# Kernel tuning notes

Measured on AMD Instinct MI355X. Metric: run time of the kernel, lower is better.

Reference implementation:

```python
import jax, jax.numpy as jnp
import numpy as np

H, KV, HD = 16, 8, 128           # heads, kv heads, head_dim
THETA, EPS = 1.0e6, 1e-6         # rope theta, rmsnorm eps
QMAX = 127.0                     # symmetric int8


def qdq(x):
    """Symmetric int8 fake quant-dequant along last dim (per-token / per-out-channel)."""
    s = jnp.maximum(jnp.max(jnp.abs(x), axis=-1, keepdims=True) / QMAX, 1e-8)
    q = jnp.clip(jnp.round(x / s), -QMAX, QMAX) * s
    return x + jax.lax.stop_gradient(q - x)  # STE


def rms_norm(x, w):
    v = jnp.mean(jnp.square(x.astype(jnp.float32)), axis=-1, keepdims=True)
    return (x.astype(jnp.float32) * jax.lax.rsqrt(v + EPS)).astype(x.dtype) * w


def rotate_half(x):
    x1, x2 = jnp.split(x, 2, axis=-1)
    return jnp.concatenate([-x2, x1], axis=-1)


def setup_inputs() -> dict:
    key = jax.random.key(0)
    ks = jax.random.split(key, 6)
    B, S, D = 1, 2048, 2048
    return {
        "hidden_states": jax.random.normal(ks[0], (B, S, D), jnp.float32),
        "Wq": jax.random.normal(ks[1], (H * HD, D), jnp.float32) * 0.02,
        "Wk": jax.random.normal(ks[2], (KV * HD, D), jnp.float32) * 0.02,
        "Wv": jax.random.normal(ks[3], (KV * HD, D), jnp.float32) * 0.02,
        "Wo": jax.random.normal(ks[4], (D, H * HD), jnp.float32) * 0.02,
        "q_norm_w": jnp.ones((HD,), jnp.float32),
        "k_norm_w": jnp.ones((HD,), jnp.float32),
        "position_ids": jnp.arange(S, dtype=jnp.int32)[None, :],
    }


def reference(hidden_states, Wq, Wk, Wv, Wo, q_norm_w, k_norm_w, position_ids):
    B, S, D = hidden_states.shape
    xq = qdq(hidden_states)                                  # per-token act quant (shared input)
    q = (xq @ qdq(Wq).T).reshape(B, S, H, HD).transpose(0, 2, 1, 3)   # [B,H,S,hd]
    k = (xq @ qdq(Wk).T).reshape(B, S, KV, HD).transpose(0, 2, 1, 3)  # [B,KV,S,hd]
    v = (xq @ qdq(Wv).T).reshape(B, S, KV, HD).transpose(0, 2, 1, 3)

    q = rms_norm(q, q_norm_w)
    k = rms_norm(k, k_norm_w)

    # rotary embeddings
    inv = 1.0 / (THETA ** (jnp.arange(0, HD, 2, dtype=jnp.float32) / HD))
    freqs = position_ids.astype(jnp.float32)[..., None] * inv          # [B,S,hd/2]
    emb = jnp.concatenate([freqs, freqs], axis=-1)                     # [B,S,hd]
    cos = jnp.cos(emb)[:, None].astype(q.dtype)                        # [B,1,S,hd]
    sin = jnp.sin(emb)[:, None].astype(q.dtype)
    q = q * cos + rotate_half(q) * sin
    k = k * cos + rotate_half(k) * sin

    # qkt_matmul.quant_x1 / quant_x2
    q = qdq(q)
    k = qdq(k)

    # GQA repeat
    g = H // KV
    k = jnp.repeat(k, g, axis=1)
    v = jnp.repeat(v, g, axis=1)

    scores = jnp.einsum("bhqd,bhkd->bhqk", q, k) * (HD ** -0.5)       # [B,H,S,S]
    causal = jnp.tril(jnp.ones((S, S), bool))
    scores = jnp.where(causal[None, None], scores, jnp.float32(-1e9))
    p = jax.nn.softmax(scores.astype(jnp.float32), axis=-1).astype(q.dtype)

    # pv_matmul.quant_x1 / quant_x2
    p = qdq(p)
    v = qdq(v)
    attn = jnp.einsum("bhqk,bhkd->bhqd", p, v)                        # [B,H,S,hd]
    attn = attn.transpose(0, 2, 1, 3).reshape(B, S, H * HD)
    return qdq(attn) @ qdq(Wo).T
```

## Files before the change

### kernel.cpp

```cpp
#include <hip/hip_runtime.h>
#include <math.h>

#define NH 16
#define NKV 8
#define HDIM 128
#define SEQ 2048
#define DMODEL 2048

typedef int   v4i __attribute__((ext_vector_type(4)));
typedef float v4f __attribute__((ext_vector_type(4)));
typedef _Float16 v8h __attribute__((ext_vector_type(8)));

static constexpr float SM_SCALE = 0.08838834764831843f;

#define GLOBP(p) (__attribute__((address_space(1))) void*)(p)
#define LDSP(p)  (__attribute__((address_space(3))) void*)(p)
#define ASYNC16(g, l) __builtin_amdgcn_global_load_lds(GLOBP(g), LDSP(l), 16, 0, 0)


__device__ __forceinline__ unsigned short f2h_bits(float x) {
    _Float16 h = (_Float16)x;
    return __builtin_bit_cast(unsigned short, h);
}

__global__ __launch_bounds__(256) void quant_rope_k(const float* __restrict__ hidden,
        const float* __restrict__ Wq, const float* __restrict__ Wk,
        const float* __restrict__ Wv, const float* __restrict__ Wo,
        const int* __restrict__ pos_ids,
        signed char* __restrict__ out, float* __restrict__ scale,
        float* __restrict__ ct, float* __restrict__ st) {
    int p = blockIdx.x;
    if (p >= 512) {
        int t = (p - 512) * 4 + (threadIdx.x >> 6);
        int fi = threadIdx.x & 63;
        float inv = 1.0f / (float)pow(1.0e6, (double)fi / 64.0);
        float fr = (float)pos_ids[t] * inv;
        float sn, c;
        sincosf(fr, &sn, &c);
        ct[t * 64 + fi] = c;
        st[t * 64 + fi] = sn;
        return;
    }
    int row0g = p * 16;
    const float* in; int lr0;
    if (row0g < 2048)      { in = hidden; lr0 = row0g; }
    else if (row0g < 4096) { in = Wq; lr0 = row0g - 2048; }
    else if (row0g < 5120) { in = Wk; lr0 = row0g - 4096; }
    else if (row0g < 6144) { in = Wv; lr0 = row0g - 5120; }
    else                   { in = Wo; lr0 = row0g - 6144; }
    const int cols = 2048;
    int tid = threadIdx.x;
    __shared__ float srow[16];
    int r = tid >> 4, l16 = tid & 15;
    const float4* x4 = (const float4*)(in + (size_t)(lr0 + r) * cols);
    float amax = 0.f;
    for (int c4 = l16; c4 < (cols >> 2); c4 += 16) {
        float4 v = x4[c4];
        amax = fmaxf(amax, fmaxf(fmaxf(fabsf(v.x), fabsf(v.y)),
                                 fmaxf(fabsf(v.z), fabsf(v.w))));
    }
#pragma unroll
    for (int m = 1; m <= 8; m <<= 1) amax = fmaxf(amax, __shfl_xor(amax, m));
    if (l16 == 0) {
        float s = fmaxf(amax / 127.0f, 1e-8f);
        srow[r] = s;
        scale[row0g + r] = s;
    }
    __syncthreads();
    int total = (cols >> 4) * 16;
    size_t obase = (size_t)p * 32768;
    for (int idx = tid; idx < total; idx += 256) {
        int f = idx >> 6, q = (idx >> 4) & 3, rr = idx & 15;
        const float* src = in + (size_t)(lr0 + rr) * cols + f * 64 + q * 16;
        float s = srow[rr];
        unsigned int wds[4];
#pragma unroll
        for (int g = 0; g < 4; ++g) {
            float4 v = *(const float4*)(src + g * 4);
            int b0 = (int)fminf(fmaxf(rintf(v.x / s), -127.f), 127.f);
            int b1 = (int)fminf(fmaxf(rintf(v.y / s), -127.f), 127.f);
            int b2 = (int)fminf(fmaxf(rintf(v.z / s), -127.f), 127.f);
            int b3 = (int)fminf(fmaxf(rintf(v.w / s), -127.f), 127.f);
            wds[g] = (b0 & 255) | ((b1 & 255) << 8) | ((b2 & 255) << 16) | ((b3 & 255) << 24);
        }
        *(uint4*)(out + obase + (size_t)idx * 16) =
            make_uint4(wds[0], wds[1], wds[2], wds[3]);
    }
}

__global__ __launch_bounds__(256) void row_quant_red_k(const float* __restrict__ attn2,
        const float* __restrict__ pp, const float* __restrict__ zb,
        signed char* __restrict__ out, float* __restrict__ scale) {
    int row0 = blockIdx.x * 16;
    bool corr = (row0 >= 1024);
    int tid = threadIdx.x;
    __shared__ float srow[16];
    __shared__ float4 spvt[16][17];
    if (corr) {
        int r = tid >> 4, h = tid & 15;
        int row = row0 + r;
        int t16 = (row >> 6) - 16, rr = row & 63;
        const float2* zb2 = (const float2*)zb;
        float2 a0 = zb2[(((size_t)h * 16 + t16) * 2 + 0) * 64 + rr];
        float2 a1 = zb2[(((size_t)h * 16 + t16) * 2 + 1) * 64 + rr];
        float M = fmaxf(a0.x, a1.x);
        float w0 = __expf(a0.x - M), w1 = __expf(a1.x - M);
        float Zt = a0.y * w0 + a1.y * w1;
        float spv = fmaxf((1.0f / Zt) / 127.0f, 1e-8f);
        spvt[r][h] = make_float4(w0, w1, spv, 0.f);
    }
    __syncthreads();
    int r = tid >> 4, l16 = tid & 15;
    int row = row0 + r;
    const float4* x4 = (const float4*)(attn2 + (size_t)row * 2048);
    size_t ppr = corr ? ((((size_t)(row >> 6) - 16) * 64 + (row & 63)) * 128) : 0;
    float amax = 0.f;
    for (int c4 = l16; c4 < 512; c4 += 16) {
        float4 v = x4[c4];
        if (corr) {
            int h = c4 >> 5;
            int j = (c4 & 31) * 4;
            float4 pv = *(const float4*)&pp[(size_t)h * 16 * 64 * 128 + ppr + j];
            float4 wz = spvt[r][h];
            v.x = (v.x * wz.x + pv.x * wz.y) * wz.z;
            v.y = (v.y * wz.x + pv.y * wz.y) * wz.z;
            v.z = (v.z * wz.x + pv.z * wz.y) * wz.z;
            v.w = (v.w * wz.x + pv.w * wz.y) * wz.z;
        }
        amax = fmaxf(amax, fmaxf(fmaxf(fabsf(v.x), fabsf(v.y)),
                                 fmaxf(fabsf(v.z), fabsf(v.w))));
    }
#pragma unroll
    for (int m = 1; m <= 8; m <<= 1) amax = fmaxf(amax, __shfl_xor(amax, m));
    if (l16 == 0) {
        float s = fmaxf(amax / 127.0f, 1e-8f);
        srow[r] = s;
        scale[row0 + r] = s;
    }
    __syncthreads();
    size_t obase = ((size_t)(row0 >> 4) * 32) << 10;
    for (int idx = tid; idx < 2048; idx += 256) {
        int f = idx >> 6, q = (idx >> 4) & 3, rr16 = idx & 15;
        int rowb = row0 + rr16;
        int colb = f * 64 + q * 16;
        const float* src = attn2 + (size_t)rowb * 2048 + colb;
        float s = srow[rr16];
        int h = f >> 1;
        float4 wz = corr ? spvt[rr16][h] : make_float4(1.f, 0.f, 0.f, 0.f);
        size_t ppb = corr ? ((size_t)h * 16 * 64 * 128
                     + (((size_t)(rowb >> 6) - 16) * 64 + (rowb & 63)) * 128 + (colb & 127)) : 0;
        unsigned int wds[4];
#pragma unroll
        for (int g = 0; g < 4; ++g) {
            float4 v = *(const float4*)(src + g * 4);
            if (corr) {
                float4 pv = *(const float4*)&pp[ppb + g * 4];
                v.x = (v.x * wz.x + pv.x * wz.y) * wz.z;
                v.y = (v.y * wz.x + pv.y * wz.y) * wz.z;
                v.z = (v.z * wz.x + pv.z * wz.y) * wz.z;
                v.w = (v.w * wz.x + pv.w * wz.y) * wz.z;
            }
            int b0 = (int)fminf(fmaxf(rintf(v.x / s), -127.f), 127.f);
            int b1 = (int)fminf(fmaxf(rintf(v.y / s), -127.f), 127.f);
            int b2 = (int)fminf(fmaxf(rintf(v.z / s), -127.f), 127.f);
            int b3 = (int)fminf(fmaxf(rintf(v.w / s), -127.f), 127.f);
            wds[g] = (b0 & 255) | ((b1 & 255) << 8) | ((b2 & 255) << 16) | ((b3 & 255) << 24);
        }
        *(uint4*)(out + obase + (size_t)idx * 16) =
            make_uint4(wds[0], wds[1], wds[2], wds[3]);
    }
}

__global__ __launch_bounds__(256, 3) void gemm_o_k(const signed char* __restrict__ A,
        const float* __restrict__ sa, const signed char* __restrict__ B,
        const float* __restrict__ sb, float* __restrict__ C, int M, int N, int K) {
    __shared__ __align__(16) signed char lsA[3][8192];
    __shared__ __align__(16) signed char lsB[3][4096];
    int tid = threadIdx.x;
    int w = tid >> 6, l = tid & 63;
    int wr = w >> 1, wc = w & 1;
    int lrow = l & 15;
    int m0 = blockIdx.y * 128, n0 = blockIdx.x * 64;
    int kb6 = K >> 6;
    v4i acc[4][2];
#pragma unroll
    for (int i = 0; i < 4; ++i)
#pragma unroll
        for (int j = 0; j < 2; ++j) acc[i][j] = (v4i){0, 0, 0, 0};

    auto stage = [&](int buf, int k6) {
#pragma unroll
        for (int a = 0; a < 2; ++a) {
            int f = a * 4 + w;
            ASYNC16(A + (((size_t)(((m0 >> 4) + f) * kb6 + k6)) << 10) + l * 16,
                    lsA[buf] + f * 1024);
        }
        ASYNC16(B + (((size_t)(((n0 >> 4) + w) * kb6 + k6)) << 10) + l * 16,
                lsB[buf] + w * 1024);
    };

    stage(0, 0);
    if (kb6 > 1) {
        stage(1, 1);
        asm volatile("s_waitcnt vmcnt(3)" ::: "memory");
    } else {
        asm volatile("s_waitcnt vmcnt(0)" ::: "memory");
    }
    __builtin_amdgcn_s_barrier();
    for (int t = 0; t < kb6; ++t) {
        if (t + 2 < kb6) stage((t + 2) % 3, t + 2);
        int cur = t % 3;
        v4i af[4], bf[2];
#pragma unroll
        for (int i = 0; i < 4; ++i) af[i] = *(const v4i*)(lsA[cur] + (wr * 4 + i) * 1024 + l * 16);
#pragma unroll
        for (int j = 0; j < 2; ++j) bf[j] = *(const v4i*)(lsB[cur] + (wc * 2 + j) * 1024 + l * 16);
#pragma unroll
        for (int i = 0; i < 4; ++i)
#pragma unroll
            for (int j = 0; j < 2; ++j)
                acc[i][j] = __builtin_amdgcn_mfma_i32_16x16x64_i8(af[i], bf[j], acc[i][j], 0, 0, 0);
        if (t + 2 < kb6) asm volatile("s_waitcnt vmcnt(3)" ::: "memory");
        else             asm volatile("s_waitcnt vmcnt(0)" ::: "memory");
        __builtin_amdgcn_s_barrier();
    }
    int r0 = m0 + wr * 64, c0 = n0 + wc * 32;
    int lg = l >> 4;
    float sbv[2];
#pragma unroll
    for (int j = 0; j < 2; ++j) sbv[j] = sb[c0 + j * 16 + lrow];
#pragma unroll
    for (int i = 0; i < 4; ++i) {
        float4 s4 = *(const float4*)(sa + r0 + i * 16 + lg * 4);
        float sav[4] = {s4.x, s4.y, s4.z, s4.w};
#pragma unroll
        for (int j = 0; j < 2; ++j) {
#pragma unroll
            for (int reg = 0; reg < 4; ++reg) {
                int rr = r0 + i * 16 + lg * 4 + reg;
                C[(size_t)rr * N + c0 + j * 16 + lrow] = (float)acc[i][j][reg] * (sav[reg] * sbv[j]);
            }
        }
    }
}

__global__ __launch_bounds__(256, 2) void gemm_qkv_k(const signed char* __restrict__ A,
        const float* __restrict__ sa, const signed char* __restrict__ B,
        const float* __restrict__ sb,
        const float* __restrict__ qw, const float* __restrict__ kw,
        const float* __restrict__ ct, const float* __restrict__ st,
        signed char* __restrict__ q_i8, float* __restrict__ sq,
        signed char* __restrict__ k_i8, float* __restrict__ sk,
        unsigned short* __restrict__ vtT) {
    __shared__ __align__(16) char smem[68608];
    signed char (*lsA)[8192] = (signed char(*)[8192])smem;
    signed char (*lsB)[8192] = (signed char(*)[8192])(smem + 24576);
    float (*tile)[132] = (float(*)[132])smem;
    float* srow = (float*)(smem + 67584);
    int tid = threadIdx.x;
    int w = tid >> 6, l = tid & 63;
    int wr = w >> 1, wc = w & 1;
    int lrow = l & 15, lg = l >> 4;
    int m0 = blockIdx.y * 128, n0 = blockIdx.x * 128;
    const int kb6 = 32;
    v4i acc[4][4];
#pragma unroll
    for (int i = 0; i < 4; ++i)
#pragma unroll
        for (int j = 0; j < 4; ++j) acc[i][j] = (v4i){0, 0, 0, 0};

    auto stage = [&](int buf, int k6) {
#pragma unroll
        for (int a = 0; a < 2; ++a) {
            int f = a * 4 + w;
            ASYNC16(A + (((size_t)(((m0 >> 4) + f) * kb6 + k6)) << 10) + l * 16,
                    lsA[buf] + f * 1024);
            ASYNC16(B + (((size_t)(((n0 >> 4) + f) * kb6 + k6)) << 10) + l * 16,
                    lsB[buf] + f * 1024);
        }
    };

    stage(0, 0);
    stage(1, 1);
    asm volatile("s_waitcnt vmcnt(4)" ::: "memory");
    __builtin_amdgcn_s_barrier();
    for (int t = 0; t < kb6; ++t) {
        if (t + 2 < kb6) stage((t + 2) % 3, t + 2);
        int cur = t % 3;
        v4i af[4], bf[4];
#pragma unroll
        for (int i = 0; i < 4; ++i) af[i] = *(const v4i*)(lsA[cur] + (wr * 4 + i) * 1024 + l * 16);
#pragma unroll
        for (int j = 0; j < 4; ++j) bf[j] = *(const v4i*)(lsB[cur] + (wc * 4 + j) * 1024 + l * 16);
#pragma unroll
        for (int i = 0; i < 4; ++i)
#pragma unroll
            for (int j = 0; j < 4; ++j)
                acc[i][j] = __builtin_amdgcn_mfma_i32_16x16x64_i8(af[i], bf[j], acc[i][j], 0, 0, 0);
        if (t + 2 < kb6) asm volatile("s_waitcnt vmcnt(4)" ::: "memory");
        else             asm volatile("s_waitcnt vmcnt(0)" ::: "memory");
        __builtin_amdgcn_s_barrier();
    }
    {
        int c0 = n0 + wc * 64;
        float sbv[4];
#pragma unroll
        for (int j = 0; j < 4; ++j) sbv[j] = sb[c0 + j * 16 + lrow];
#pragma unroll
        for (int i = 0; i < 4; ++i) {
            float4 s4 = *(const float4*)(sa + m0 + wr * 64 + i * 16 + lg * 4);
            float sav[4] = {s4.x, s4.y, s4.z, s4.w};
#pragma unroll
            for (int j = 0; j < 4; ++j)
#pragma unroll
                for (int reg = 0; reg < 4; ++reg)
                    tile[wr * 64 + i * 16 + lg * 4 + reg][wc * 64 + j * 16 + lrow] =
                        (float)acc[i][j][reg] * (sav[reg] * sbv[j]);
        }
    }
    __syncthreads();
    int slot = n0 >> 7;
    if (slot < 24) {
        const float* wn = (slot < 16) ? qw : kw;
        signed char* dst8 = (slot < 16) ? q_i8 + (size_t)slot * (SEQ * 128)
                                        : k_i8 + (size_t)(slot - 16) * (SEQ * 128);
        float* sdst = (slot < 16) ? sq + (size_t)slot * SEQ : sk + (size_t)(slot - 16) * SEQ;
        float wn0 = wn[l], wn1 = wn[l + 64];
        for (int it = 0; it < 32; ++it) {
            int tl = it * 4 + w;
            int t = m0 + tl;
            float x0 = tile[tl][l];
            float x1 = tile[tl][l + 64];
            float ss = x0 * x0 + x1 * x1;
#pragma unroll
            for (int m = 1; m <= 32; m <<= 1) ss += __shfl_xor(ss, m);
            float rs = 1.0f / sqrtf(ss / 128.0f + 1e-6f);
            x0 = (x0 * rs) * wn0;
            x1 = (x1 * rs) * wn1;
            float cth = ct[t * 64 + l];
            float sth = st[t * 64 + l];
            float nx0 = x0 * cth - x1 * sth;
            float nx1 = x1 * cth + x0 * sth;
            float amax = fmaxf(fabsf(nx0), fabsf(nx1));
#pragma unroll
            for (int m = 1; m <= 32; m <<= 1) amax = fmaxf(amax, __shfl_xor(amax, m));
            float s = fmaxf(amax / 127.0f, 1e-8f);
            float q0 = fminf(fmaxf(rintf(nx0 / s), -127.f), 127.f);
            float q1 = fminf(fmaxf(rintf(nx1 / s), -127.f), 127.f);
            size_t ta0 = (size_t)(((t >> 4) * 2) << 10)
                       + (size_t)((((l >> 4) & 3) << 8) + ((t & 15) << 4) + (l & 15));
            dst8[ta0] = (signed char)(int)q0;
            dst8[ta0 + 1024] = (signed char)(int)q1;
            if (l == 0) sdst[t] = s;
        }
    } else {
        int kv = slot - 24;
        for (int it = 0; it < 32; ++it) {
            int tl = it * 4 + w;
            float x0 = tile[tl][l];
            float x1 = tile[tl][l + 64];
            float amax = fmaxf(fabsf(x0), fabsf(x1));
#pragma unroll
            for (int m = 1; m <= 32; m <<= 1) amax = fmaxf(amax, __shfl_xor(amax, m));
            if (l == 0) srow[tl] = fmaxf(amax / 127.0f, 1e-8f);
        }
        __syncthreads();
        int d = tid >> 1, th = (tid & 1) * 32;
        size_t base = (size_t)kv * (SEQ * 128);
#pragma unroll
        for (int kbl = 0; kbl < 2; ++kbl) {
            int kb = (m0 >> 6) + kbl;
#pragma unroll
            for (int j = 0; j < 32; j += 2) {
                int t64 = th + j;
                int tg = kbl * 64 + t64;
                float s0 = srow[tg], s1 = srow[tg + 1];
                float a = fminf(fmaxf(rintf(tile[tg][d] / s0), -127.f), 127.f) * s0;
                float b = fminf(fmaxf(rintf(tile[tg + 1][d] / s1), -127.f), 127.f) * s1;
                unsigned int ua = f2h_bits(a), ub = f2h_bits(b);
                int off = kb * 8192 + ((d >> 4) * 2 + ((t64 >> 5) & 1)) * 512
                        + (((d & 15) + (((t64 >> 3) & 3) << 4)) << 3) + (t64 & 7);
                *(unsigned int*)(vtT + base + off) = ua | (ub << 16);
            }
        }
    }
}

__global__ __launch_bounds__(256, 2) void attn_k(const signed char* __restrict__ q_i8,
        const float* __restrict__ sq, const signed char* __restrict__ k_i8,
        const float* __restrict__ sk, const unsigned short* __restrict__ vtT,
        float* __restrict__ attn2, float* __restrict__ pp, float* __restrict__ zb) {
    __shared__ __align__(16) unsigned short vlds[3][8192];
    __shared__ __align__(16) signed char klds[2][8192];
    __shared__ __align__(16) unsigned short plds[4096];
    __shared__ __align__(16) float slds[1024];
    int bx = blockIdx.x, hp = blockIdx.y;
    int qb = 31 - (bx >> 1), c = bx & 1;
    int nch2 = (qb >= 16) ? 2 : 1;
    if (c >= nch2) return;
    int q0 = qb * 64;
    int kb0 = c * 16, kb1 = min((c + 1) * 16, qb + 1);
    int tid = threadIdx.x, w = tid >> 6, l = tid & 63;
    int lrow = l & 15, lg = l >> 4;
    int h0 = hp * 2, h1 = h0 + 1;

    const signed char* qtA = q_i8 + (size_t)h0 * (SEQ * 128)
                           + ((size_t)((((q0 >> 4) + w) * 2)) << 10) + l * 16;
    const signed char* qtB = qtA + (size_t)(SEQ * 128);
    v4i qfA0 = *(const v4i*)(qtA), qfA1 = *(const v4i*)(qtA + 1024);
    v4i qfB0 = *(const v4i*)(qtB), qfB1 = *(const v4i*)(qtB + 1024);
    float4 sA = *(const float4*)(sq + (size_t)h0 * SEQ + q0 + w * 16 + lg * 4);
    float4 sB = *(const float4*)(sq + (size_t)h1 * SEQ + q0 + w * 16 + lg * 4);
    float sqrA[4] = {sA.x, sA.y, sA.z, sA.w};
    float sqrB[4] = {sB.x, sB.y, sB.z, sB.w};

    const signed char* kbase = k_i8 + (size_t)hp * (SEQ * 128);
    const float* skb = sk + (size_t)hp * SEQ;
    const unsigned short* vt = vtT + (size_t)hp * (SEQ * 128);

    auto issueV = [&](int kb) {
        unsigned short* vb = &vlds[kb % 3][0];
#pragma unroll
        for (int a = 0; a < 4; ++a) {
            int fv = a * 4 + w;
            ASYNC16(vt + (size_t)kb * 8192 + fv * 512 + l * 8, vb + fv * 512);
        }
    };
    auto issueK = [&](int kb) {
        signed char* kbuf = &klds[kb & 1][0];
#pragma unroll
        for (int a = 0; a < 2; ++a) {
            int f = a * 4 + w;
            ASYNC16(kbase + ((size_t)(kb * 8 + f) << 10) + l * 16, kbuf + f * 1024);
        }
    };

    v4f accA[8], accB[8];
#pragma unroll
    for (int jd = 0; jd < 8; ++jd) {
        accA[jd] = (v4f){0.f, 0.f, 0.f, 0.f};
        accB[jd] = (v4f){0.f, 0.f, 0.f, 0.f};
    }
    float ztA[4] = {0.f, 0.f, 0.f, 0.f};
    float ztB[4] = {0.f, 0.f, 0.f, 0.f};
    float mA[4], mB[4];
#pragma unroll
    for (int r = 0; r < 4; ++r) { mA[r] = -1e30f; mB[r] = -1e30f; }

    ASYNC16(skb + kb0 * 64 + w * 256 + l * 4, (char*)slds + w * 1024);
    issueK(kb0);
    issueV(kb0);
    if (kb0 + 1 < kb1) {
        issueV(kb0 + 1);
        asm volatile("s_waitcnt vmcnt(4)" ::: "memory");
    } else {
        asm volatile("s_waitcnt vmcnt(0)" ::: "memory");
    }
    __builtin_amdgcn_s_barrier();

    for (int kb = kb0; kb < kb1; ++kb) {
        int k0 = kb * 64;
        if (kb + 1 < kb1) issueK(kb + 1);
        if (kb + 2 < kb1) issueV(kb + 2);
        v4i ka[8];
#pragma unroll
        for (int f = 0; f < 8; ++f)
            ka[f] = *(const v4i*)(&klds[kb & 1][0] + f * 1024 + l * 16);
        float skc[4];
#pragma unroll
        for (int j = 0; j < 4; ++j) skc[j] = slds[(kb - kb0) * 64 + j * 16 + lrow];
        v4i sciA[4], sciB[4];
#pragma unroll
        for (int j = 0; j < 4; ++j) {
            v4i z = {0, 0, 0, 0};
            v4i tA = __builtin_amdgcn_mfma_i32_16x16x64_i8(qfA0, ka[j * 2], z, 0, 0, 0);
            sciA[j] = __builtin_amdgcn_mfma_i32_16x16x64_i8(qfA1, ka[j * 2 + 1], tA, 0, 0, 0);
            v4i tB = __builtin_amdgcn_mfma_i32_16x16x64_i8(qfB0, ka[j * 2], z, 0, 0, 0);
            sciB[j] = __builtin_amdgcn_mfma_i32_16x16x64_i8(qfB1, ka[j * 2 + 1], tB, 0, 0, 0);
        }
        float svA[4][4], svB[4][4];
        float tmA[4], tmB[4];
#pragma unroll
        for (int reg = 0; reg < 4; ++reg) { tmA[reg] = -1e30f; tmB[reg] = -1e30f; }
#pragma unroll
        for (int reg = 0; reg < 4; ++reg) {
            int r = q0 + w * 16 + lg * 4 + reg;
#pragma unroll
            for (int j = 0; j < 4; ++j) {
                int cc = j * 16 + lrow;
                bool ok = (k0 + cc <= r);
                float ss = skc[j] * SM_SCALE;
                svA[reg][j] = ok ? ((float)sciA[j][reg] * sqrA[reg]) * ss : -1e30f;
                svB[reg][j] = ok ? ((float)sciB[j][reg] * sqrB[reg]) * ss : -1e30f;
                tmA[reg] = fmaxf(tmA[reg], svA[reg][j]);
                tmB[reg] = fmaxf(tmB[reg], svB[reg][j]);
            }
        }
#pragma unroll
        for (int reg = 0; reg < 4; ++reg) {
#pragma unroll
            for (int mask = 1; mask <= 8; mask <<= 1) {
                tmA[reg] = fmaxf(tmA[reg], __shfl_xor(tmA[reg], mask));
                tmB[reg] = fmaxf(tmB[reg], __shfl_xor(tmB[reg], mask));
            }
        }
        float efA[4], efB[4];
#pragma unroll
        for (int reg = 0; reg < 4; ++reg) {
            float mnA = fmaxf(mA[reg], tmA[reg]);
            efA[reg] = __expf(mA[reg] - mnA);
            mA[reg] = mnA;
            ztA[reg] *= efA[reg];
            float mnB = fmaxf(mB[reg], tmB[reg]);
            efB[reg] = __expf(mB[reg] - mnB);
            mB[reg] = mnB;
            ztB[reg] *= efB[reg];
        }
        v4f efvA = {efA[0], efA[1], efA[2], efA[3]};
        v4f efvB = {efB[0], efB[1], efB[2], efB[3]};
#pragma unroll
        for (int jd = 0; jd < 8; ++jd) {
            accA[jd] *= efvA;
            accB[jd] *= efvB;
        }
#pragma unroll
        for (int reg = 0; reg < 4; ++reg) {
            int rq = lg * 4 + reg;
#pragma unroll
            for (int j = 0; j < 4; ++j) {
                int cc = j * 16 + lrow;
                float pd = 0.f;
                float sv = svA[reg][j];
                if (sv > -5e29f) {
                    float e = __expf(sv - mA[reg]);
                    ztA[reg] += e;
                    pd = fminf(rintf(127.0f * e), 127.f);
                }
                plds[(w * 2 + (cc >> 5)) * 512 + (rq + 16 * ((cc >> 3) & 3)) * 8 + (cc & 7)] =
                    f2h_bits(pd);
            }
        }
        v8h pfA0 = *(const v8h*)(plds + (w * 2 + 0) * 512 + l * 8);
        v8h pfA1 = *(const v8h*)(plds + (w * 2 + 1) * 512 + l * 8);
#pragma unroll
        for (int reg = 0; reg < 4; ++reg) {
            int rq = lg * 4 + reg;
#pragma unroll
            for (int j = 0; j < 4; ++j) {
                int cc = j * 16 + lrow;
                float pd = 0.f;
                float sv = svB[reg][j];
                if (sv > -5e29f) {
                    float e = __expf(sv - mB[reg]);
                    ztB[reg] += e;
                    pd = fminf(rintf(127.0f * e), 127.f);
                }
                plds[(w * 2 + (cc >> 5)) * 512 + (rq + 16 * ((cc >> 3) & 3)) * 8 + (cc & 7)] =
                    f2h_bits(pd);
            }
        }
        v8h pfB0 = *(const v8h*)(plds + (w * 2 + 0) * 512 + l * 8);
        v8h pfB1 = *(const v8h*)(plds + (w * 2 + 1) * 512 + l * 8);
        const unsigned short* vb = &vlds[kb % 3][0];
#pragma unroll
        for (int jd = 0; jd < 8; ++jd) {
            v8h vh0 = *(const v8h*)(vb + (jd * 2 + 0) * 512 + l * 8);
            v8h vh1 = *(const v8h*)(vb + (jd * 2 + 1) * 512 + l * 8);
            v4f tA = accA[jd];
            tA = __builtin_amdgcn_mfma_f32_16x16x32_f16(pfA0, vh0, tA, 0, 0, 0);
            tA = __builtin_amdgcn_mfma_f32_16x16x32_f16(pfA1, vh1, tA, 0, 0, 0);
            accA[jd] = tA;
            v4f tB = accB[jd];
            tB = __builtin_amdgcn_mfma_f32_16x16x32_f16(pfB0, vh0, tB, 0, 0, 0);
            tB = __builtin_amdgcn_mfma_f32_16x16x32_f16(pfB1, vh1, tB, 0, 0, 0);
            accB[jd] = tB;
        }
        if (kb + 2 < kb1) asm volatile("s_waitcnt vmcnt(4)" ::: "memory");
        else              asm volatile("s_waitcnt vmcnt(0)" ::: "memory");
        __builtin_amdgcn_s_barrier();
    }
#pragma unroll
    for (int reg = 0; reg < 4; ++reg) {
#pragma unroll
        for (int mask = 1; mask <= 8; mask <<= 1) {
            ztA[reg] += __shfl_xor(ztA[reg], mask);
            ztB[reg] += __shfl_xor(ztB[reg], mask);
        }
    }
    if (qb < 16) {
        float spA[4], spB[4];
#pragma unroll
        for (int reg = 0; reg < 4; ++reg) {
            spA[reg] = fmaxf((1.0f / ztA[reg]) / 127.0f, 1e-8f);
            spB[reg] = fmaxf((1.0f / ztB[reg]) / 127.0f, 1e-8f);
        }
#pragma unroll
        for (int jd = 0; jd < 8; ++jd)
#pragma unroll
            for (int reg = 0; reg < 4; ++reg) {
                int r = q0 + w * 16 + lg * 4 + reg;
                attn2[(size_t)r * DMODEL + h0 * HDIM + jd * 16 + lrow] = accA[jd][reg] * spA[reg];
                attn2[(size_t)r * DMODEL + h1 * HDIM + jd * 16 + lrow] = accB[jd][reg] * spB[reg];
            }
    } else {
        if (c == 0) {
#pragma unroll
            for (int jd = 0; jd < 8; ++jd)
#pragma unroll
                for (int reg = 0; reg < 4; ++reg) {
                    int r = q0 + w * 16 + lg * 4 + reg;
                    attn2[(size_t)r * DMODEL + h0 * HDIM + jd * 16 + lrow] = accA[jd][reg];
                    attn2[(size_t)r * DMODEL + h1 * HDIM + jd * 16 + lrow] = accB[jd][reg];
                }
        } else {
#pragma unroll
            for (int jd = 0; jd < 8; ++jd)
#pragma unroll
                for (int reg = 0; reg < 4; ++reg) {
                    int rr = w * 16 + lg * 4 + reg;
                    pp[(((size_t)h0 * 16 + (qb - 16)) * 64 + rr) * 128 + jd * 16 + lrow] = accA[jd][reg];
                    pp[(((size_t)h1 * 16 + (qb - 16)) * 64 + rr) * 128 + jd * 16 + lrow] = accB[jd][reg];
                }
        }
        if (lrow == 0) {
            float2* zb2 = (float2*)zb;
            size_t zA = (((size_t)h0 * 16 + (qb - 16)) * 2 + c) * 64;
            size_t zB = (((size_t)h1 * 16 + (qb - 16)) * 2 + c) * 64;
#pragma unroll
            for (int reg = 0; reg < 4; ++reg) {
                zb2[zA + w * 16 + lg * 4 + reg] = make_float2(mA[reg], ztA[reg]);
                zb2[zB + w * 16 + lg * 4 + reg] = make_float2(mB[reg], ztB[reg]);
            }
        }
    }
}

extern "C" void kernel_launch(void* const* d_in, const int* in_sizes, int n_in,
                              void* d_out, int out_size, void* d_ws, size_t ws_size,
                              hipStream_t stream) {
    (void)in_sizes; (void)n_in; (void)out_size; (void)ws_size;
    const float* hidden = (const float*)d_in[0];
    const float* Wq = (const float*)d_in[1];
    const float* Wk = (const float*)d_in[2];
    const float* Wv = (const float*)d_in[3];
    const float* Wo = (const float*)d_in[4];
    const float* qw = (const float*)d_in[5];
    const float* kw = (const float*)d_in[6];
    const int* pos = (const int*)d_in[7];
    float* out = (float*)d_out;
    char* ws = (char*)d_ws;

    const size_t MB = 1024 * 1024;
    signed char* x_i8  = (signed char*)(ws);
    signed char* wq_i8 = (signed char*)(ws + 4 * MB);
    signed char* wo_i8 = (signed char*)(ws + 12 * MB);
    signed char* q_i8  = (signed char*)(ws + 16 * MB);
    signed char* k_i8  = (signed char*)(ws + 20 * MB);
    float* sx  = (float*)(ws + 22 * MB);
    float* swq = sx + 2048;
    float* swo = sx + 6144;
    float* sq  = sx + 8192;
    float* sk  = sq + NH * SEQ;
    float* sa  = sk + NKV * SEQ;
    float* ct  = (float*)(ws + 22 * MB + 512 * 1024);
    float* st  = (float*)(ws + 22 * MB + 1024 * 1024);
    float* attn2 = (float*)(ws + 32 * MB);
    float* pp    = (float*)(ws + 48 * MB);
    unsigned short* vtT = (unsigned short*)(ws + 56 * MB);
    float* zb    = (float*)(ws + 60 * MB);
    signed char* a_i8 = x_i8;

    quant_rope_k<<<1024, 256, 0, stream>>>(hidden, Wq, Wk, Wv, Wo, pos, x_i8, sx, ct, st);

    gemm_qkv_k<<<dim3(32, 16), 256, 0, stream>>>(x_i8, sx, wq_i8, swq, qw, kw, ct, st,
                                                 q_i8, sq, k_i8, sk, vtT);

    attn_k<<<dim3(64, 8), 256, 0, stream>>>(q_i8, sq, k_i8, sk, vtT, attn2, pp, zb);

    row_quant_red_k<<<128, 256, 0, stream>>>(attn2, pp, zb, a_i8, sa);
    gemm_o_k<<<dim3(32, 16), 256, 0, stream>>>(a_i8, sa, wo_i8, swo, out, 2048, 2048, 2048);
}
```

Measured before the change: 187.0 us.

## Split every attention query block's KV range into two balanced halves

Before, only query blocks 16 and above were split across two workgroups, and always at kv block 16, which left the work uneven. Now every query block's causal KV range is cut at its midpoint, so both workgroups get roughly equal work. A workgroup with an empty range writes neutral softmax stats and exits. The reduction kernel now always merges two partials per row, which adds pp reads and writes for every row, and the workspace layout is resized to hold the larger partial buffers.

```diff
diff --git a/kernel.cpp b/kernel.cpp
--- a/kernel.cpp
+++ b/kernel.cpp
@@ -92,17 +92,16 @@
         const float* __restrict__ pp, const float* __restrict__ zb,
         signed char* __restrict__ out, float* __restrict__ scale) {
     int row0 = blockIdx.x * 16;
-    bool corr = (row0 >= 1024);
     int tid = threadIdx.x;
     __shared__ float srow[16];
     __shared__ float4 spvt[16][17];
-    if (corr) {
+    {
         int r = tid >> 4, h = tid & 15;
         int row = row0 + r;
-        int t16 = (row >> 6) - 16, rr = row & 63;
+        int t32 = row >> 6, rr = row & 63;
         const float2* zb2 = (const float2*)zb;
-        float2 a0 = zb2[(((size_t)h * 16 + t16) * 2 + 0) * 64 + rr];
-        float2 a1 = zb2[(((size_t)h * 16 + t16) * 2 + 1) * 64 + rr];
+        float2 a0 = zb2[(((size_t)h * 32 + t32) * 2 + 0) * 64 + rr];
+        float2 a1 = zb2[(((size_t)h * 32 + t32) * 2 + 1) * 64 + rr];
         float M = fmaxf(a0.x, a1.x);
         float w0 = __expf(a0.x - M), w1 = __expf(a1.x - M);
         float Zt = a0.y * w0 + a1.y * w1;
@@ -113,20 +112,18 @@
     int r = tid >> 4, l16 = tid & 15;
     int row = row0 + r;
     const float4* x4 = (const float4*)(attn2 + (size_t)row * 2048);
-    size_t ppr = corr ? ((((size_t)(row >> 6) - 16) * 64 + (row & 63)) * 128) : 0;
+    size_t ppr = ((size_t)(row >> 6) * 64 + (row & 63)) * 128;
     float amax = 0.f;
     for (int c4 = l16; c4 < 512; c4 += 16) {
         float4 v = x4[c4];
-        if (corr) {
-            int h = c4 >> 5;
-            int j = (c4 & 31) * 4;
-            float4 pv = *(const float4*)&pp[(size_t)h * 16 * 64 * 128 + ppr + j];
-            float4 wz = spvt[r][h];
-            v.x = (v.x * wz.x + pv.x * wz.y) * wz.z;
-            v.y = (v.y * wz.x + pv.y * wz.y) * wz.z;
-            v.z = (v.z * wz.x + pv.z * wz.y) * wz.z;
-            v.w = (v.w * wz.x + pv.w * wz.y) * wz.z;
-        }
+        int h = c4 >> 5;
+        int j = (c4 & 31) * 4;
+        float4 pv = *(const float4*)&pp[(size_t)h * 32 * 64 * 128 + ppr + j];
+        float4 wz = spvt[r][h];
+        v.x = (v.x * wz.x + pv.x * wz.y) * wz.z;
+        v.y = (v.y * wz.x + pv.y * wz.y) * wz.z;
+        v.z = (v.z * wz.x + pv.z * wz.y) * wz.z;
+        v.w = (v.w * wz.x + pv.w * wz.y) * wz.z;
         amax = fmaxf(amax, fmaxf(fmaxf(fabsf(v.x), fabsf(v.y)),
                                  fmaxf(fabsf(v.z), fabsf(v.w))));
     }
@@ -146,20 +143,18 @@
         const float* src = attn2 + (size_t)rowb * 2048 + colb;
         float s = srow[rr16];
         int h = f >> 1;
-        float4 wz = corr ? spvt[rr16][h] : make_float4(1.f, 0.f, 0.f, 0.f);
-        size_t ppb = corr ? ((size_t)h * 16 * 64 * 128
-                     + (((size_t)(rowb >> 6) - 16) * 64 + (rowb & 63)) * 128 + (colb & 127)) : 0;
+        float4 wz = spvt[rr16][h];
+        size_t ppb = (size_t)h * 32 * 64 * 128
+                   + ((size_t)(rowb >> 6) * 64 + (rowb & 63)) * 128 + (colb & 127);
         unsigned int wds[4];
 #pragma unroll
         for (int g = 0; g < 4; ++g) {
             float4 v = *(const float4*)(src + g * 4);
-            if (corr) {
-                float4 pv = *(const float4*)&pp[ppb + g * 4];
-                v.x = (v.x * wz.x + pv.x * wz.y) * wz.z;
-                v.y = (v.y * wz.x + pv.y * wz.y) * wz.z;
-                v.z = (v.z * wz.x + pv.z * wz.y) * wz.z;
-                v.w = (v.w * wz.x + pv.w * wz.y) * wz.z;
-            }
+            float4 pv = *(const float4*)&pp[ppb + g * 4];
+            v.x = (v.x * wz.x + pv.x * wz.y) * wz.z;
+            v.y = (v.y * wz.x + pv.y * wz.y) * wz.z;
+            v.z = (v.z * wz.x + pv.z * wz.y) * wz.z;
+            v.w = (v.w * wz.x + pv.w * wz.y) * wz.z;
             int b0 = (int)fminf(fmaxf(rintf(v.x / s), -127.f), 127.f);
             int b1 = (int)fminf(fmaxf(rintf(v.y / s), -127.f), 127.f);
             int b2 = (int)fminf(fmaxf(rintf(v.z / s), -127.f), 127.f);
@@ -396,13 +391,27 @@
     __shared__ __align__(16) float slds[1024];
     int bx = blockIdx.x, hp = blockIdx.y;
     int qb = 31 - (bx >> 1), c = bx & 1;
-    int nch2 = (qb >= 16) ? 2 : 1;
-    if (c >= nch2) return;
     int q0 = qb * 64;
-    int kb0 = c * 16, kb1 = min((c + 1) * 16, qb + 1);
+    int hsp = (qb + 2) >> 1;
+    int kb0 = c ? hsp : 0;
+    int kb1 = c ? (qb + 1) : hsp;
     int tid = threadIdx.x, w = tid >> 6, l = tid & 63;
     int lrow = l & 15, lg = l >> 4;
     int h0 = hp * 2, h1 = h0 + 1;
+
+    if (kb0 >= kb1) {
+        if (lrow == 0) {
+            float2* zb2 = (float2*)zb;
+            size_t zA = (((size_t)h0 * 32 + qb) * 2 + c) * 64;
+            size_t zB = (((size_t)h1 * 32 + qb) * 2 + c) * 64;
+#pragma unroll
+            for (int reg = 0; reg < 4; ++reg) {
+                zb2[zA + w * 16 + lg * 4 + reg] = make_float2(-1e30f, 0.f);
+                zb2[zB + w * 16 + lg * 4 + reg] = make_float2(-1e30f, 0.f);
+            }
+        }
+        return;
+    }
 
     const signed char* qtA = q_i8 + (size_t)h0 * (SEQ * 128)
                            + ((size_t)((((q0 >> 4) + w) * 2)) << 10) + l * 16;
@@ -587,50 +596,33 @@
             ztB[reg] += __shfl_xor(ztB[reg], mask);
         }
     }
-    if (qb < 16) {
-        float spA[4], spB[4];
-#pragma unroll
-        for (int reg = 0; reg < 4; ++reg) {
-            spA[reg] = fmaxf((1.0f / ztA[reg]) / 127.0f, 1e-8f);
-            spB[reg] = fmaxf((1.0f / ztB[reg]) / 127.0f, 1e-8f);
-        }
+    if (c == 0) {
 #pragma unroll
         for (int jd = 0; jd < 8; ++jd)
 #pragma unroll
             for (int reg = 0; reg < 4; ++reg) {
                 int r = q0 + w * 16 + lg * 4 + reg;
-                attn2[(size_t)r * DMODEL + h0 * HDIM + jd * 16 + lrow] = accA[jd][reg] * spA[reg];
-                attn2[(size_t)r * DMODEL + h1 * HDIM + jd * 16 + lrow] = accB[jd][reg] * spB[reg];
+                attn2[(size_t)r * DMODEL + h0 * HDIM + jd * 16 + lrow] = accA[jd][reg];
+                attn2[(size_t)r * DMODEL + h1 * HDIM + jd * 16 + lrow] = accB[jd][reg];
             }
     } else {
-        if (c == 0) {
-#pragma unroll
-            for (int jd = 0; jd < 8; ++jd)
-#pragma unroll
-                for (int reg = 0; reg < 4; ++reg) {
-                    int r = q0 + w * 16 + lg * 4 + reg;
-                    attn2[(size_t)r * DMODEL + h0 * HDIM + jd * 16 + lrow] = accA[jd][reg];
-                    attn2[(size_t)r * DMODEL + h1 * HDIM + jd * 16 + lrow] = accB[jd][reg];
-                }
-        } else {
-#pragma unroll
-            for (int jd = 0; jd < 8; ++jd)
-#pragma unroll
-                for (int reg = 0; reg < 4; ++reg) {
-                    int rr = w * 16 + lg * 4 + reg;
-                    pp[(((size_t)h0 * 16 + (qb - 16)) * 64 + rr) * 128 + jd * 16 + lrow] = accA[jd][reg];
-                    pp[(((size_t)h1 * 16 + (qb - 16)) * 64 + rr) * 128 + jd * 16 + lrow] = accB[jd][reg];
-                }
-        }
-        if (lrow == 0) {
-            float2* zb2 = (float2*)zb;
-            size_t zA = (((size_t)h0 * 16 + (qb - 16)) * 2 + c) * 64;
-            size_t zB = (((size_t)h1 * 16 + (qb - 16)) * 2 + c) * 64;
+#pragma unroll
+        for (int jd = 0; jd < 8; ++jd)
 #pragma unroll
             for (int reg = 0; reg < 4; ++reg) {
-                zb2[zA + w * 16 + lg * 4 + reg] = make_float2(mA[reg], ztA[reg]);
-                zb2[zB + w * 16 + lg * 4 + reg] = make_float2(mB[reg], ztB[reg]);
-            }
+                int rr = w * 16 + lg * 4 + reg;
+                pp[(((size_t)h0 * 32 + qb) * 64 + rr) * 128 + jd * 16 + lrow] = accA[jd][reg];
+                pp[(((size_t)h1 * 32 + qb) * 64 + rr) * 128 + jd * 16 + lrow] = accB[jd][reg];
+            }
+    }
+    if (lrow == 0) {
+        float2* zb2 = (float2*)zb;
+        size_t zA = (((size_t)h0 * 32 + qb) * 2 + c) * 64;
+        size_t zB = (((size_t)h1 * 32 + qb) * 2 + c) * 64;
+#pragma unroll
+        for (int reg = 0; reg < 4; ++reg) {
+            zb2[zA + w * 16 + lg * 4 + reg] = make_float2(mA[reg], ztA[reg]);
+            zb2[zB + w * 16 + lg * 4 + reg] = make_float2(mB[reg], ztB[reg]);
         }
     }
 }
@@ -664,10 +656,10 @@
     float* sa  = sk + NKV * SEQ;
     float* ct  = (float*)(ws + 22 * MB + 512 * 1024);
     float* st  = (float*)(ws + 22 * MB + 1024 * 1024);
-    float* attn2 = (float*)(ws + 32 * MB);
-    float* pp    = (float*)(ws + 48 * MB);
-    unsigned short* vtT = (unsigned short*)(ws + 56 * MB);
-    float* zb    = (float*)(ws + 60 * MB);
+    unsigned short* vtT = (unsigned short*)(ws + 24 * MB);
+    float* zb    = (float*)(ws + 28 * MB);
+    float* attn2 = (float*)(ws + 30 * MB);
+    float* pp    = (float*)(ws + 46 * MB);
     signed char* a_i8 = x_i8;
 
     quant_rope_k<<<1024, 256, 0, stream>>>(hidden, Wq, Wk, Wv, Wo, pos, x_i8, sx, ct, st);
```

Result: faster. 179.3 us (-4.1%).
